# Performance work log

Measured on AMD Instinct MI355X. Metric: run time of the kernel, lower is better.

Reference implementation:

```python
import jax, jax.numpy as jnp
import numpy as np

B = 32768; NF = 8; E = 16; V = 100000; D = 4
IN = 2 * NF * E          # 256 = id_dims + agn_dims
FCN = [256, 128, 64]
DIMS = [IN] + FCN
EPS = 1e-5               # BatchNorm1d eps


def setup_inputs() -> dict:
    ks = jax.random.split(jax.random.key(0), 64)
    inp = {
        'id_idx': jax.random.randint(ks[0], (B, NF), 0, V),
        'agn_idx': jax.random.randint(ks[1], (B, NF), 0, V),
        'domain_id': jax.random.randint(ks[2], (B,), 0, D),
        'id_tables': jax.random.normal(ks[3], (NF, V, E), dtype=jnp.float32) * 0.01,
        'agn_tables': jax.random.normal(ks[4], (NF, V, E), dtype=jnp.float32) * 0.01,
    }
    k = 5
    for i in range(len(FCN)):
        din, dout = DIMS[i], DIMS[i + 1]
        inp[f'mlp_W{i}'] = jax.random.normal(ks[k], (D, din, dout), dtype=jnp.float32) / np.sqrt(din).astype(np.float32); k += 1
        inp[f'mlp_b{i}'] = jnp.zeros((D, dout), jnp.float32)
        inp[f'bn_g{i}'] = jnp.ones((D, dout), jnp.float32)
        inp[f'bn_b{i}'] = jnp.zeros((D, dout), jnp.float32)
        inp[f'gate_W1_{i}'] = jax.random.normal(ks[k], (D, IN, dout), dtype=jnp.float32) / np.sqrt(IN).astype(np.float32); k += 1
        inp[f'gate_b1_{i}'] = jnp.zeros((D, dout), jnp.float32)
        inp[f'gate_W2_{i}'] = jax.random.normal(ks[k], (D, dout, dout), dtype=jnp.float32) / np.sqrt(dout).astype(np.float32); k += 1
        inp[f'gate_b2_{i}'] = jnp.zeros((D, dout), jnp.float32)
    inp['fin_W'] = jax.random.normal(ks[k], (D, DIMS[-1], 1), dtype=jnp.float32) / np.sqrt(DIMS[-1]).astype(np.float32)
    inp['fin_b'] = jnp.zeros((D, 1), jnp.float32)
    return inp


def _embed(tables, idx):
    # tables [NF,V,E], idx [B,NF] -> [B, NF*E] (per-feature lookup then concat)
    g = tables[jnp.arange(NF)[None, :], idx]            # [B,NF,E]
    return g.reshape(idx.shape[0], NF * E)


def _ppnet(id_tables, agn_tables, mlp_W, mlp_b, bn_g, bn_b, gW1, gb1, gW2, gb2,
           fin_W, fin_b, id_idx, agn_idx, domain_id):
    id_x = _embed(id_tables, id_idx)                    # [B, 128]
    agn_x = _embed(agn_tables, agn_idx)                 # [B, 128]
    # gate_input = cat(id_x, agn_x.detach())
    gate_in = jnp.concatenate([id_x, jax.lax.stop_gradient(agn_x)], axis=1)  # [B, IN]
    h = None
    for i in range(len(FCN)):
        # GateNU: Linear->ReLU->Linear->2*sigmoid, broadcast over D domain towers
        g1 = jax.nn.relu(jnp.einsum('bi,dio->dbo', gate_in, gW1[i]) + gb1[i][:, None, :])
        gate = 2.0 * jax.nn.sigmoid(jnp.einsum('dbo,dop->dbp', g1, gW2[i]) + gb2[i][:, None, :])
        # MLP layer: Linear -> BatchNorm1d (train-mode batch stats) -> ReLU
        if h is None:
            h = jnp.einsum('bi,dio->dbo', gate_in, mlp_W[i]) + mlp_b[i][:, None, :]
        else:
            h = jnp.einsum('dbi,dio->dbo', h, mlp_W[i]) + mlp_b[i][:, None, :]
        mu = h.mean(axis=1, keepdims=True)
        var = h.var(axis=1, keepdims=True)              # biased, matches torch BN training
        h = (h - mu) * jax.lax.rsqrt(var + EPS) * bn_g[i][:, None, :] + bn_b[i][:, None, :]
        h = jax.nn.relu(h)
        h = h * gate
    out = jax.nn.sigmoid(jnp.einsum('dbh,dho->dbo', h, fin_W) + fin_b[:, None, :])  # [D,B,1]
    out = out[:, :, 0]                                  # [D,B]
    # torch.where masked-select chain == gather the row of the assigned domain
    return out[domain_id, jnp.arange(out.shape[1])]     # [B]


def reference(id_idx, agn_idx, domain_id, id_tables, agn_tables,
              mlp_W0, mlp_b0, bn_g0, bn_b0, gate_W1_0, gate_b1_0, gate_W2_0, gate_b2_0,
              mlp_W1, mlp_b1, bn_g1, bn_b1, gate_W1_1, gate_b1_1, gate_W2_1, gate_b2_1,
              mlp_W2, mlp_b2, bn_g2, bn_b2, gate_W1_2, gate_b1_2, gate_W2_2, gate_b2_2,
              fin_W, fin_b):
    mlp_W = [mlp_W0, mlp_W1, mlp_W2]; mlp_b = [mlp_b0, mlp_b1, mlp_b2]
    bn_g = [bn_g0, bn_g1, bn_g2]; bn_b = [bn_b0, bn_b1, bn_b2]
    gW1 = [gate_W1_0, gate_W1_1, gate_W1_2]; gb1 = [gate_b1_0, gate_b1_1, gate_b1_2]
    gW2 = [gate_W2_0, gate_W2_1, gate_W2_2]; gb2 = [gate_b2_0, gate_b2_1, gate_b2_2]
    return _ppnet(id_tables, agn_tables, mlp_W, mlp_b, bn_g, bn_b, gW1, gb1, gW2, gb2,
                  fin_W, fin_b, id_idx, agn_idx, domain_id)
```

## Files before the change

### kernel.cpp

```cpp
#include <hip/hip_runtime.h>


typedef __attribute__((ext_vector_type(8))) short short8;
typedef __attribute__((ext_vector_type(4))) float floatx4;

#define BATCH 32768
#define NDOM 4
#define TM 64

__device__ __forceinline__ unsigned short f2b(float f) {
    unsigned u = __float_as_uint(f);
    u += 0x7fffu + ((u >> 16) & 1u);
    return (unsigned short)(u >> 16);
}
__device__ __forceinline__ float b2f(unsigned short h) {
    return __uint_as_float(((unsigned)h) << 16);
}

struct MatDesc { const float* src; unsigned K, N, pfx, total; };
struct PrepArgs { MatDesc m[9]; float* stats; unsigned statsN; unsigned grand; };

__global__ __launch_bounds__(256) void prep_k(PrepArgs a, unsigned short* __restrict__ wt) {
    unsigned e = blockIdx.x * 256 + threadIdx.x;
    if (e < a.statsN) a.stats[e] = 0.f;
    if (e >= a.grand) return;
    int j = 0;
    while (j < 8 && e >= a.m[j].pfx + a.m[j].total) j++;
    const unsigned K = a.m[j].K, N = a.m[j].N;
    const unsigned local = e - a.m[j].pfx;
    const unsigned kn = K * N;
    const unsigned d = local / kn;
    const unsigned r2 = local - d * kn;
    const unsigned n = r2 / K;
    const unsigned k = r2 - n * K;
    wt[e] = f2b(a.m[j].src[((long long)d * K + k) * N + n]);
}

__global__ __launch_bounds__(256) void embed_k(const int* __restrict__ idi, const int* __restrict__ agi,
                                               const float* __restrict__ idt, const float* __restrict__ agt,
                                               unsigned short* __restrict__ gin) {
    int t = blockIdx.x * 256 + threadIdx.x;
    int b = t >> 4, slot = t & 15;
    int f = slot & 7;
    const int* ip = (slot < 8) ? idi : agi;
    const float* tab = (slot < 8) ? idt : agt;
    int ix = ip[b * 8 + f];
    const float* src = tab + ((long long)f * 100000 + ix) * 16;
    unsigned short tmp[16];
#pragma unroll
    for (int j = 0; j < 16; j++) tmp[j] = f2b(src[j]);
    unsigned short* dst = gin + (long long)b * 256 + slot * 16;
    *(uint4*)dst = *(const uint4*)tmp;
    *(uint4*)(dst + 8) = *(const uint4*)(tmp + 8);
}

template <int N, int KX>
__global__ __launch_bounds__(256, 2) void stats_k(
    const unsigned short* __restrict__ X, int ginMode,
    const unsigned short* __restrict__ Wm,
    float* __restrict__ gsum, float* __restrict__ gssq) {
    constexpr int GX = KX / 8;
    constexpr int NW = N / 4, CT = NW / 16;
    __shared__ __align__(16) unsigned short tA[TM * KX];
    const int t = threadIdx.x;
    const int d = blockIdx.y;
    const int m0 = blockIdx.x * TM;
    const unsigned short* Xp = X + ((long long)(ginMode ? 0 : d * BATCH) + m0) * KX;
#pragma unroll
    for (int r = 0; r < TM * GX / 256; r++) {
        int idx = r * 256 + t;
        int m = idx / GX, j = idx % GX;
        uint4 v = *(const uint4*)(Xp + (long long)m * KX + j * 8);
        *(uint4*)&tA[(m * GX + (j ^ (m & 7))) * 8] = v;
    }
    __syncthreads();
    const int w = t >> 6, lane = t & 63, lrow = lane & 15, lq = lane >> 4;
    const int n0w = w * NW;
    const unsigned short* Wp = Wm + ((long long)d * N + n0w) * KX;
    floatx4 acc[4][CT];
#pragma unroll
    for (int rt = 0; rt < 4; rt++)
#pragma unroll
        for (int ct = 0; ct < CT; ct++) acc[rt][ct] = (floatx4)(0.f);
#pragma unroll
    for (int k0 = 0; k0 < KX; k0 += 32) {
        short8 a[4], b[CT];
#pragma unroll
        for (int rt = 0; rt < 4; rt++) {
            int m = rt * 16 + lrow;
            a[rt] = *(const short8*)&tA[(m * GX + (((k0 >> 3) | lq) ^ (m & 7))) * 8];
        }
#pragma unroll
        for (int ct = 0; ct < CT; ct++)
            b[ct] = *(const short8*)(Wp + (long long)(ct * 16 + lrow) * KX + k0 + lq * 8);
#pragma unroll
        for (int rt = 0; rt < 4; rt++)
#pragma unroll
            for (int ct = 0; ct < CT; ct++)
                acc[rt][ct] = __builtin_amdgcn_mfma_f32_16x16x32_bf16(a[rt], b[ct], acc[rt][ct], 0, 0, 0);
    }
#pragma unroll
    for (int ct = 0; ct < CT; ct++) {
        float s = 0.f, ss = 0.f;
#pragma unroll
        for (int rt = 0; rt < 4; rt++)
#pragma unroll
            for (int r = 0; r < 4; r++) { float v = acc[rt][ct][r]; s += v; ss += v * v; }
        s += __shfl_down(s, 32); ss += __shfl_down(ss, 32);
        s += __shfl_down(s, 16); ss += __shfl_down(ss, 16);
        if (lane < 16) {
            atomicAdd(&gsum[d * N + n0w + ct * 16 + lane], s);
            atomicAdd(&gssq[d * N + n0w + ct * 16 + lane], ss);
        }
    }
}

__global__ void fin_k(const float* __restrict__ gsum, const float* __restrict__ gssq,
                      const float* __restrict__ gma, const float* __restrict__ bta,
                      float* __restrict__ SC, float* __restrict__ SH, int total, float invB) {
    int i = blockIdx.x * blockDim.x + threadIdx.x;
    if (i >= total) return;
    float ma = gsum[i] * invB;
    float var = gssq[i] * invB - ma * ma;
    float rs = rsqrtf(var + 1e-5f);
    float sc = rs * gma[i];
    SC[i] = sc;
    SH[i] = bta[i] - ma * sc;
}

template <int N, int KX, bool RESTAGE, bool FINAL>
__global__ __launch_bounds__(256, 2) void fused_k(
    const unsigned short* __restrict__ gin,
    const unsigned short* __restrict__ Xh,
    const unsigned short* __restrict__ W1,
    const unsigned short* __restrict__ W2,
    const unsigned short* __restrict__ Wm,
    const float* __restrict__ gb1, const float* __restrict__ gb2,
    const float* __restrict__ SC, const float* __restrict__ SH,
    unsigned short* __restrict__ Xn,
    const int* __restrict__ dom, const float* __restrict__ fw,
    const float* __restrict__ fb, float* __restrict__ outp) {
    constexpr int GG = N / 8;
    constexpr int GX = KX / 8;
    constexpr int NW = N / 4, CT = NW / 16;
    __shared__ __align__(16) unsigned short tA[TM * 256];
    __shared__ __align__(16) unsigned short g1b[TM * N];
    const int t = threadIdx.x;
    const int d = blockIdx.y;
    const int m0 = blockIdx.x * TM;
    const int w = t >> 6, lane = t & 63, lrow = lane & 15, lq = lane >> 4;
    const int n0w = w * NW;

    {
        const unsigned short* Gp = gin + (long long)m0 * 256;
#pragma unroll
        for (int r = 0; r < 8; r++) {
            int idx = r * 256 + t;
            int m = idx >> 5, j = idx & 31;
            uint4 v = *(const uint4*)(Gp + (long long)m * 256 + j * 8);
            *(uint4*)&tA[((m << 5) + (j ^ (m & 7))) * 8] = v;
        }
    }
    __syncthreads();

    floatx4 acc1[4][CT];
#pragma unroll
    for (int rt = 0; rt < 4; rt++)
#pragma unroll
        for (int ct = 0; ct < CT; ct++) acc1[rt][ct] = (floatx4)(0.f);
    const unsigned short* W1p = W1 + ((long long)d * N + n0w) * 256;
#pragma unroll
    for (int k0 = 0; k0 < 256; k0 += 32) {
        short8 a[4], b[CT];
#pragma unroll
        for (int rt = 0; rt < 4; rt++) {
            int m = rt * 16 + lrow;
            a[rt] = *(const short8*)&tA[((m << 5) + (((k0 >> 3) | lq) ^ (m & 7))) * 8];
        }
#pragma unroll
        for (int ct = 0; ct < CT; ct++)
            b[ct] = *(const short8*)(W1p + (long long)(ct * 16 + lrow) * 256 + k0 + lq * 8);
#pragma unroll
        for (int rt = 0; rt < 4; rt++)
#pragma unroll
            for (int ct = 0; ct < CT; ct++)
                acc1[rt][ct] = __builtin_amdgcn_mfma_f32_16x16x32_bf16(a[rt], b[ct], acc1[rt][ct], 0, 0, 0);
    }
#pragma unroll
    for (int ct = 0; ct < CT; ct++) {
        int n = n0w + ct * 16 + lrow;
        float bs = gb1[d * N + n];
        int jj = n >> 3, sub = n & 7;
#pragma unroll
        for (int rt = 0; rt < 4; rt++)
#pragma unroll
            for (int r = 0; r < 4; r++) {
                int m = rt * 16 + lq * 4 + r;
                g1b[(m * GG + (jj ^ (m & 7))) * 8 + sub] = f2b(fmaxf(acc1[rt][ct][r] + bs, 0.f));
            }
    }
    __syncthreads();

    floatx4 acc2[4][CT];
#pragma unroll
    for (int rt = 0; rt < 4; rt++)
#pragma unroll
        for (int ct = 0; ct < CT; ct++) acc2[rt][ct] = (floatx4)(0.f);
    const unsigned short* W2p = W2 + ((long long)d * N + n0w) * N;
#pragma unroll
    for (int k0 = 0; k0 < N; k0 += 32) {
        short8 a[4], b[CT];
#pragma unroll
        for (int rt = 0; rt < 4; rt++) {
            int m = rt * 16 + lrow;
            a[rt] = *(const short8*)&g1b[(m * GG + (((k0 >> 3) | lq) ^ (m & 7))) * 8];
        }
#pragma unroll
        for (int ct = 0; ct < CT; ct++)
            b[ct] = *(const short8*)(W2p + (long long)(ct * 16 + lrow) * N + k0 + lq * 8);
#pragma unroll
        for (int rt = 0; rt < 4; rt++)
#pragma unroll
            for (int ct = 0; ct < CT; ct++)
                acc2[rt][ct] = __builtin_amdgcn_mfma_f32_16x16x32_bf16(a[rt], b[ct], acc2[rt][ct], 0, 0, 0);
    }
    float gate[4][CT][4];
#pragma unroll
    for (int ct = 0; ct < CT; ct++) {
        int n = n0w + ct * 16 + lrow;
        float bs = gb2[d * N + n];
#pragma unroll
        for (int rt = 0; rt < 4; rt++)
#pragma unroll
            for (int r = 0; r < 4; r++)
                gate[rt][ct][r] = 2.f / (1.f + __expf(-(acc2[rt][ct][r] + bs)));
    }

    if (RESTAGE) {
        const unsigned short* Xp = Xh + ((long long)d * BATCH + m0) * KX;
#pragma unroll
        for (int r = 0; r < TM * GX / 256; r++) {
            int idx = r * 256 + t;
            int m = idx / GX, j = idx % GX;
            uint4 v = *(const uint4*)(Xp + (long long)m * KX + j * 8);
            *(uint4*)&tA[(m * GX + (j ^ (m & 7))) * 8] = v;
        }
    }
    __syncthreads();

    floatx4 acch[4][CT];
#pragma unroll
    for (int rt = 0; rt < 4; rt++)
#pragma unroll
        for (int ct = 0; ct < CT; ct++) acch[rt][ct] = (floatx4)(0.f);
    const unsigned short* Wmp = Wm + ((long long)d * N + n0w) * KX;
#pragma unroll
    for (int k0 = 0; k0 < KX; k0 += 32) {
        short8 a[4], b[CT];
#pragma unroll
        for (int rt = 0; rt < 4; rt++) {
            int m = rt * 16 + lrow;
            a[rt] = *(const short8*)&tA[(m * GX + (((k0 >> 3) | lq) ^ (m & 7))) * 8];
        }
#pragma unroll
        for (int ct = 0; ct < CT; ct++)
            b[ct] = *(const short8*)(Wmp + (long long)(ct * 16 + lrow) * KX + k0 + lq * 8);
#pragma unroll
        for (int rt = 0; rt < 4; rt++)
#pragma unroll
            for (int ct = 0; ct < CT; ct++)
                acch[rt][ct] = __builtin_amdgcn_mfma_f32_16x16x32_bf16(a[rt], b[ct], acch[rt][ct], 0, 0, 0);
    }
#pragma unroll
    for (int ct = 0; ct < CT; ct++) {
        int n = n0w + ct * 16 + lrow;
        float sc = SC[d * N + n], sh = SH[d * N + n];
#pragma unroll
        for (int rt = 0; rt < 4; rt++)
#pragma unroll
            for (int r = 0; r < 4; r++) {
                int m = rt * 16 + lq * 4 + r;
                float v = fmaxf(acch[rt][ct][r] * sc + sh, 0.f) * gate[rt][ct][r];
                g1b[m * N + n] = f2b(v);
            }
    }
    __syncthreads();

    if (!FINAL) {
        unsigned short* Op = Xn + ((long long)d * BATCH + m0) * N;
#pragma unroll
        for (int r = 0; r < TM * GG / 256; r++) {
            int idx = r * 256 + t;
            int m = idx / GG, j = idx % GG;
            *(uint4*)(Op + (long long)m * N + j * 8) = *(const uint4*)&g1b[(m * GG + j) * 8];
        }
    } else {
        int m = t >> 2, q = t & 3;
        const float* fwp = fw + d * 64;
        float s = 0.f;
#pragma unroll
        for (int k = 0; k < 16; k++) s += b2f(g1b[m * 64 + q * 16 + k]) * fwp[q * 16 + k];
        s += __shfl_down(s, 1);
        s += __shfl_down(s, 2);
        if (q == 0) {
            int b = m0 + m;
            if (dom[b] == d) outp[b] = 1.f / (1.f + __expf(-(s + fb[d])));
        }
    }
}

extern "C" void kernel_launch(void* const* d_in, const int* in_sizes, int n_in,
                              void* d_out, int out_size, void* d_ws, size_t ws_size,
                              hipStream_t stream) {
    const int B = BATCH, D = NDOM;

    const int* id_idx = (const int*)d_in[0];
    const int* agn_idx = (const int*)d_in[1];
    const int* dom = (const int*)d_in[2];
    const float* id_t = (const float*)d_in[3];
    const float* agn_t = (const float*)d_in[4];
    const float *mlpW[3], *bng[3], *bnb[3], *gW1[3], *gb1[3], *gW2[3], *gb2[3];
    for (int i = 0; i < 3; i++) {
        int b0 = 5 + i * 8;
        mlpW[i] = (const float*)d_in[b0 + 0];
        bng[i] = (const float*)d_in[b0 + 2];
        bnb[i] = (const float*)d_in[b0 + 3];
        gW1[i] = (const float*)d_in[b0 + 4];
        gb1[i] = (const float*)d_in[b0 + 5];
        gW2[i] = (const float*)d_in[b0 + 6];
        gb2[i] = (const float*)d_in[b0 + 7];
    }
    const float* finW = (const float*)d_in[29];
    const float* finb = (const float*)d_in[30];

    char* wsc = (char*)d_ws;
    size_t off = 0;
    auto alloc = [&](size_t bytes) -> char* {
        char* p = wsc + off;
        off = (off + bytes + 255) & ~(size_t)255;
        return p;
    };

    struct { const float* src; int K, N; } mats[9] = {
        {mlpW[0], 256, 256}, {gW1[0], 256, 256}, {gW2[0], 256, 256},
        {mlpW[1], 256, 128}, {gW1[1], 256, 128}, {gW2[1], 128, 128},
        {mlpW[2], 128, 64},  {gW1[2], 256, 64},  {gW2[2], 64, 64}};
    unsigned pfx[10];
    pfx[0] = 0;
    for (int j = 0; j < 9; j++) pfx[j + 1] = pfx[j] + 4u * mats[j].K * mats[j].N;

    unsigned short* wt = (unsigned short*)alloc((size_t)pfx[9] * 2);
    unsigned short* gin = (unsigned short*)alloc((size_t)B * 256 * 2);
    float* stats = (float*)alloc((size_t)3 * 2 * D * 256 * 4);
    float* scsh = (float*)alloc((size_t)3 * 2 * D * 256 * 4);
    unsigned short* X1 = (unsigned short*)alloc((size_t)D * B * 256 * 2);
    unsigned short* X2 = (unsigned short*)alloc((size_t)D * B * 128 * 2);

    PrepArgs pa;
    for (int j = 0; j < 9; j++) {
        pa.m[j].src = mats[j].src;
        pa.m[j].K = (unsigned)mats[j].K;
        pa.m[j].N = (unsigned)mats[j].N;
        pa.m[j].pfx = pfx[j];
        pa.m[j].total = 4u * mats[j].K * mats[j].N;
    }
    pa.stats = stats;
    pa.statsN = 3 * 2 * D * 256;
    pa.grand = pfx[9];

    const float invB = 1.f / (float)B;
    dim3 gs(B / TM, D);

    prep_k<<<dim3((pfx[9] + 255) / 256), 256, 0, stream>>>(pa, wt);
    embed_k<<<dim3(B * 16 / 256), 256, 0, stream>>>(id_idx, agn_idx, id_t, agn_t, gin);

    float* gsum0 = stats + 0 * 2 * D * 256; float* gssq0 = gsum0 + D * 256;
    float* gsum1 = stats + 1 * 2 * D * 256; float* gssq1 = gsum1 + D * 256;
    float* gsum2 = stats + 2 * 2 * D * 256; float* gssq2 = gsum2 + D * 256;
    float* SC0 = scsh + 0 * 2 * D * 256; float* SH0 = SC0 + D * 256;
    float* SC1 = scsh + 1 * 2 * D * 256; float* SH1 = SC1 + D * 256;
    float* SC2 = scsh + 2 * 2 * D * 256; float* SH2 = SC2 + D * 256;

    stats_k<256, 256><<<gs, 256, 0, stream>>>(gin, 1, wt + pfx[0], gsum0, gssq0);
    fin_k<<<(D * 256 + 255) / 256, 256, 0, stream>>>(gsum0, gssq0, bng[0], bnb[0], SC0, SH0, D * 256, invB);
    fused_k<256, 256, false, false><<<gs, 256, 0, stream>>>(
        gin, gin, wt + pfx[1], wt + pfx[2], wt + pfx[0], gb1[0], gb2[0], SC0, SH0,
        X1, nullptr, nullptr, nullptr, nullptr);

    stats_k<128, 256><<<gs, 256, 0, stream>>>(X1, 0, wt + pfx[3], gsum1, gssq1);
    fin_k<<<(D * 128 + 255) / 256, 256, 0, stream>>>(gsum1, gssq1, bng[1], bnb[1], SC1, SH1, D * 128, invB);
    fused_k<128, 256, true, false><<<gs, 256, 0, stream>>>(
        gin, X1, wt + pfx[4], wt + pfx[5], wt + pfx[3], gb1[1], gb2[1], SC1, SH1,
        X2, nullptr, nullptr, nullptr, nullptr);

    stats_k<64, 128><<<gs, 256, 0, stream>>>(X2, 0, wt + pfx[6], gsum2, gssq2);
    fin_k<<<(D * 64 + 255) / 256, 256, 0, stream>>>(gsum2, gssq2, bng[2], bnb[2], SC2, SH2, D * 64, invB);
    fused_k<64, 128, true, true><<<gs, 256, 0, stream>>>(
        gin, X2, wt + pfx[7], wt + pfx[8], wt + pfx[6], gb1[2], gb2[2], SC2, SH2,
        nullptr, dom, finW, finb, (float*)d_out);
}
```

Before: 506.7 us.

## Fuse next-layer BN statistics and BN finalize into fused layer kernels

Folds the per-layer BatchNorm statistics GEMM for layers 1 and 2 into the previous layer's fused kernel, which now runs the next layer's pre-BN matmul on the output tile still in LDS and accumulates sums via shared-memory atomics before global atomics. BN scale/shift finalization moves into each fused kernel's prologue, and the separate stats and fin kernels for later layers are removed. This avoids re-reading X1/X2 from memory and cuts several launches. In exchange, the fused kernels reuse one shared buffer with extra barriers, pack gates into bf16 registers, and raise launch bounds to 3 blocks per SM, which adds work per block and register pressure.

```diff
diff --git a/kernel.cpp b/kernel.cpp
--- a/kernel.cpp
+++ b/kernel.cpp
@@ -54,18 +54,16 @@
     *(uint4*)(dst + 8) = *(const uint4*)(tmp + 8);
 }
 
-template <int N, int KX>
-__global__ __launch_bounds__(256, 2) void stats_k(
-    const unsigned short* __restrict__ X, int ginMode,
+__global__ __launch_bounds__(256, 3) void stats_k(
+    const unsigned short* __restrict__ X,
     const unsigned short* __restrict__ Wm,
     float* __restrict__ gsum, float* __restrict__ gssq) {
-    constexpr int GX = KX / 8;
-    constexpr int NW = N / 4, CT = NW / 16;
+    constexpr int N = 256, KX = 256, GX = KX / 8, CT = 4;
     __shared__ __align__(16) unsigned short tA[TM * KX];
     const int t = threadIdx.x;
     const int d = blockIdx.y;
     const int m0 = blockIdx.x * TM;
-    const unsigned short* Xp = X + ((long long)(ginMode ? 0 : d * BATCH) + m0) * KX;
+    const unsigned short* Xp = X + (long long)m0 * KX;
 #pragma unroll
     for (int r = 0; r < TM * GX / 256; r++) {
         int idx = r * 256 + t;
@@ -75,7 +73,7 @@
     }
     __syncthreads();
     const int w = t >> 6, lane = t & 63, lrow = lane & 15, lq = lane >> 4;
-    const int n0w = w * NW;
+    const int n0w = w * 64;
     const unsigned short* Wp = Wm + ((long long)d * N + n0w) * KX;
     floatx4 acc[4][CT];
 #pragma unroll
@@ -115,41 +113,43 @@
     }
 }
 
-__global__ void fin_k(const float* __restrict__ gsum, const float* __restrict__ gssq,
-                      const float* __restrict__ gma, const float* __restrict__ bta,
-                      float* __restrict__ SC, float* __restrict__ SH, int total, float invB) {
-    int i = blockIdx.x * blockDim.x + threadIdx.x;
-    if (i >= total) return;
-    float ma = gsum[i] * invB;
-    float var = gssq[i] * invB - ma * ma;
-    float rs = rsqrtf(var + 1e-5f);
-    float sc = rs * gma[i];
-    SC[i] = sc;
-    SH[i] = bta[i] - ma * sc;
-}
-
-template <int N, int KX, bool RESTAGE, bool FINAL>
-__global__ __launch_bounds__(256, 2) void fused_k(
+template <int N, int KX, int NN, bool GINH, bool FINAL>
+__global__ __launch_bounds__(256, 3) void fused_k(
     const unsigned short* __restrict__ gin,
     const unsigned short* __restrict__ Xh,
     const unsigned short* __restrict__ W1,
     const unsigned short* __restrict__ W2,
     const unsigned short* __restrict__ Wm,
+    const unsigned short* __restrict__ WmN,
     const float* __restrict__ gb1, const float* __restrict__ gb2,
-    const float* __restrict__ SC, const float* __restrict__ SH,
+    const float* __restrict__ gsum, const float* __restrict__ gssq,
+    const float* __restrict__ gma, const float* __restrict__ bta,
+    float* __restrict__ gsumN, float* __restrict__ gssqN,
     unsigned short* __restrict__ Xn,
     const int* __restrict__ dom, const float* __restrict__ fw,
-    const float* __restrict__ fb, float* __restrict__ outp) {
-    constexpr int GG = N / 8;
+    const float* __restrict__ fb, float* __restrict__ outp, float invB) {
+    constexpr int GGn = N / 8;
     constexpr int GX = KX / 8;
-    constexpr int NW = N / 4, CT = NW / 16;
-    __shared__ __align__(16) unsigned short tA[TM * 256];
-    __shared__ __align__(16) unsigned short g1b[TM * N];
+    constexpr int CT = N / 64;
+    constexpr int CTn = (NN > 0) ? (NN / 64) : 1;
+    __shared__ __align__(16) unsigned short buf[TM * 256];
+    __shared__ float sSC[N], sSH[N];
+    __shared__ float sSum[NN > 0 ? NN : 1], sSsq[NN > 0 ? NN : 1];
+
     const int t = threadIdx.x;
     const int d = blockIdx.y;
     const int m0 = blockIdx.x * TM;
     const int w = t >> 6, lane = t & 63, lrow = lane & 15, lq = lane >> 4;
-    const int n0w = w * NW;
+    const int n0w = w * (N / 4);
+
+    if (t < N) {
+        float ma = gsum[d * N + t] * invB;
+        float var = gssq[d * N + t] * invB - ma * ma;
+        float sc = rsqrtf(var + 1e-5f) * gma[d * N + t];
+        sSC[t] = sc;
+        sSH[t] = bta[d * N + t] - ma * sc;
+    }
+    if (NN > 0 && t < NN) { sSum[t] = 0.f; sSsq[t] = 0.f; }
 
     {
         const unsigned short* Gp = gin + (long long)m0 * 256;
@@ -158,7 +158,7 @@
             int idx = r * 256 + t;
             int m = idx >> 5, j = idx & 31;
             uint4 v = *(const uint4*)(Gp + (long long)m * 256 + j * 8);
-            *(uint4*)&tA[((m << 5) + (j ^ (m & 7))) * 8] = v;
+            *(uint4*)&buf[((m << 5) + (j ^ (m & 7))) * 8] = v;
         }
     }
     __syncthreads();
@@ -168,24 +168,27 @@
     for (int rt = 0; rt < 4; rt++)
 #pragma unroll
         for (int ct = 0; ct < CT; ct++) acc1[rt][ct] = (floatx4)(0.f);
-    const unsigned short* W1p = W1 + ((long long)d * N + n0w) * 256;
-#pragma unroll
-    for (int k0 = 0; k0 < 256; k0 += 32) {
-        short8 a[4], b[CT];
-#pragma unroll
-        for (int rt = 0; rt < 4; rt++) {
-            int m = rt * 16 + lrow;
-            a[rt] = *(const short8*)&tA[((m << 5) + (((k0 >> 3) | lq) ^ (m & 7))) * 8];
-        }
-#pragma unroll
-        for (int ct = 0; ct < CT; ct++)
-            b[ct] = *(const short8*)(W1p + (long long)(ct * 16 + lrow) * 256 + k0 + lq * 8);
-#pragma unroll
-        for (int rt = 0; rt < 4; rt++)
+    {
+        const unsigned short* W1p = W1 + ((long long)d * N + n0w) * 256;
+#pragma unroll
+        for (int k0 = 0; k0 < 256; k0 += 32) {
+            short8 a[4], b[CT];
+#pragma unroll
+            for (int rt = 0; rt < 4; rt++) {
+                int m = rt * 16 + lrow;
+                a[rt] = *(const short8*)&buf[((m << 5) + (((k0 >> 3) | lq) ^ (m & 7))) * 8];
+            }
 #pragma unroll
             for (int ct = 0; ct < CT; ct++)
-                acc1[rt][ct] = __builtin_amdgcn_mfma_f32_16x16x32_bf16(a[rt], b[ct], acc1[rt][ct], 0, 0, 0);
-    }
+                b[ct] = *(const short8*)(W1p + (long long)(ct * 16 + lrow) * 256 + k0 + lq * 8);
+#pragma unroll
+            for (int rt = 0; rt < 4; rt++)
+#pragma unroll
+                for (int ct = 0; ct < CT; ct++)
+                    acc1[rt][ct] = __builtin_amdgcn_mfma_f32_16x16x32_bf16(a[rt], b[ct], acc1[rt][ct], 0, 0, 0);
+        }
+    }
+    __syncthreads();
 #pragma unroll
     for (int ct = 0; ct < CT; ct++) {
         int n = n0w + ct * 16 + lrow;
@@ -196,7 +199,7 @@
 #pragma unroll
             for (int r = 0; r < 4; r++) {
                 int m = rt * 16 + lq * 4 + r;
-                g1b[(m * GG + (jj ^ (m & 7))) * 8 + sub] = f2b(fmaxf(acc1[rt][ct][r] + bs, 0.f));
+                buf[(m * GGn + (jj ^ (m & 7))) * 8 + sub] = f2b(fmaxf(acc1[rt][ct][r] + bs, 0.f));
             }
     }
     __syncthreads();
@@ -206,44 +209,51 @@
     for (int rt = 0; rt < 4; rt++)
 #pragma unroll
         for (int ct = 0; ct < CT; ct++) acc2[rt][ct] = (floatx4)(0.f);
-    const unsigned short* W2p = W2 + ((long long)d * N + n0w) * N;
-#pragma unroll
-    for (int k0 = 0; k0 < N; k0 += 32) {
-        short8 a[4], b[CT];
-#pragma unroll
-        for (int rt = 0; rt < 4; rt++) {
-            int m = rt * 16 + lrow;
-            a[rt] = *(const short8*)&g1b[(m * GG + (((k0 >> 3) | lq) ^ (m & 7))) * 8];
-        }
-#pragma unroll
-        for (int ct = 0; ct < CT; ct++)
-            b[ct] = *(const short8*)(W2p + (long long)(ct * 16 + lrow) * N + k0 + lq * 8);
-#pragma unroll
-        for (int rt = 0; rt < 4; rt++)
+    {
+        const unsigned short* W2p = W2 + ((long long)d * N + n0w) * N;
+#pragma unroll
+        for (int k0 = 0; k0 < N; k0 += 32) {
+            short8 a[4], b[CT];
+#pragma unroll
+            for (int rt = 0; rt < 4; rt++) {
+                int m = rt * 16 + lrow;
+                a[rt] = *(const short8*)&buf[(m * GGn + ((((k0 >> 3) | lq)) ^ (m & 7))) * 8];
+            }
 #pragma unroll
             for (int ct = 0; ct < CT; ct++)
-                acc2[rt][ct] = __builtin_amdgcn_mfma_f32_16x16x32_bf16(a[rt], b[ct], acc2[rt][ct], 0, 0, 0);
-    }
-    float gate[4][CT][4];
+                b[ct] = *(const short8*)(W2p + (long long)(ct * 16 + lrow) * N + k0 + lq * 8);
+#pragma unroll
+            for (int rt = 0; rt < 4; rt++)
+#pragma unroll
+                for (int ct = 0; ct < CT; ct++)
+                    acc2[rt][ct] = __builtin_amdgcn_mfma_f32_16x16x32_bf16(a[rt], b[ct], acc2[rt][ct], 0, 0, 0);
+        }
+    }
+    unsigned gatep[4][CT][2];
 #pragma unroll
     for (int ct = 0; ct < CT; ct++) {
         int n = n0w + ct * 16 + lrow;
         float bs = gb2[d * N + n];
 #pragma unroll
-        for (int rt = 0; rt < 4; rt++)
-#pragma unroll
-            for (int r = 0; r < 4; r++)
-                gate[rt][ct][r] = 2.f / (1.f + __expf(-(acc2[rt][ct][r] + bs)));
-    }
-
-    if (RESTAGE) {
-        const unsigned short* Xp = Xh + ((long long)d * BATCH + m0) * KX;
+        for (int rt = 0; rt < 4; rt++) {
+            float g0 = 2.f / (1.f + __expf(-(acc2[rt][ct][0] + bs)));
+            float g1 = 2.f / (1.f + __expf(-(acc2[rt][ct][1] + bs)));
+            float g2 = 2.f / (1.f + __expf(-(acc2[rt][ct][2] + bs)));
+            float g3 = 2.f / (1.f + __expf(-(acc2[rt][ct][3] + bs)));
+            gatep[rt][ct][0] = (unsigned)f2b(g0) | ((unsigned)f2b(g1) << 16);
+            gatep[rt][ct][1] = (unsigned)f2b(g2) | ((unsigned)f2b(g3) << 16);
+        }
+    }
+    __syncthreads();
+
+    {
+        const unsigned short* Xp = Xh + ((long long)(GINH ? 0 : d * BATCH) + m0) * KX;
 #pragma unroll
         for (int r = 0; r < TM * GX / 256; r++) {
             int idx = r * 256 + t;
             int m = idx / GX, j = idx % GX;
             uint4 v = *(const uint4*)(Xp + (long long)m * KX + j * 8);
-            *(uint4*)&tA[(m * GX + (j ^ (m & 7))) * 8] = v;
+            *(uint4*)&buf[(m * GX + (j ^ (m & 7))) * 8] = v;
         }
     }
     __syncthreads();
@@ -253,58 +263,117 @@
     for (int rt = 0; rt < 4; rt++)
 #pragma unroll
         for (int ct = 0; ct < CT; ct++) acch[rt][ct] = (floatx4)(0.f);
-    const unsigned short* Wmp = Wm + ((long long)d * N + n0w) * KX;
-#pragma unroll
-    for (int k0 = 0; k0 < KX; k0 += 32) {
-        short8 a[4], b[CT];
-#pragma unroll
-        for (int rt = 0; rt < 4; rt++) {
-            int m = rt * 16 + lrow;
-            a[rt] = *(const short8*)&tA[(m * GX + (((k0 >> 3) | lq) ^ (m & 7))) * 8];
-        }
-#pragma unroll
-        for (int ct = 0; ct < CT; ct++)
-            b[ct] = *(const short8*)(Wmp + (long long)(ct * 16 + lrow) * KX + k0 + lq * 8);
-#pragma unroll
-        for (int rt = 0; rt < 4; rt++)
+    {
+        const unsigned short* Wmp = Wm + ((long long)d * N + n0w) * KX;
+#pragma unroll
+        for (int k0 = 0; k0 < KX; k0 += 32) {
+            short8 a[4], b[CT];
+#pragma unroll
+            for (int rt = 0; rt < 4; rt++) {
+                int m = rt * 16 + lrow;
+                a[rt] = *(const short8*)&buf[(m * GX + (((k0 >> 3) | lq) ^ (m & 7))) * 8];
+            }
 #pragma unroll
             for (int ct = 0; ct < CT; ct++)
-                acch[rt][ct] = __builtin_amdgcn_mfma_f32_16x16x32_bf16(a[rt], b[ct], acch[rt][ct], 0, 0, 0);
-    }
+                b[ct] = *(const short8*)(Wmp + (long long)(ct * 16 + lrow) * KX + k0 + lq * 8);
+#pragma unroll
+            for (int rt = 0; rt < 4; rt++)
+#pragma unroll
+                for (int ct = 0; ct < CT; ct++)
+                    acch[rt][ct] = __builtin_amdgcn_mfma_f32_16x16x32_bf16(a[rt], b[ct], acch[rt][ct], 0, 0, 0);
+        }
+    }
+    __syncthreads();
+
 #pragma unroll
     for (int ct = 0; ct < CT; ct++) {
         int n = n0w + ct * 16 + lrow;
-        float sc = SC[d * N + n], sh = SH[d * N + n];
-#pragma unroll
-        for (int rt = 0; rt < 4; rt++)
+        float sc = sSC[n], sh = sSH[n];
+        int jj = n >> 3, sub = n & 7;
+#pragma unroll
+        for (int rt = 0; rt < 4; rt++) {
+            float gv[4] = {b2f((unsigned short)(gatep[rt][ct][0] & 0xffff)),
+                           b2f((unsigned short)(gatep[rt][ct][0] >> 16)),
+                           b2f((unsigned short)(gatep[rt][ct][1] & 0xffff)),
+                           b2f((unsigned short)(gatep[rt][ct][1] >> 16))};
 #pragma unroll
             for (int r = 0; r < 4; r++) {
                 int m = rt * 16 + lq * 4 + r;
-                float v = fmaxf(acch[rt][ct][r] * sc + sh, 0.f) * gate[rt][ct][r];
-                g1b[m * N + n] = f2b(v);
-            }
+                float v = fmaxf(acch[rt][ct][r] * sc + sh, 0.f) * gv[r];
+                buf[(m * GGn + (jj ^ (m & 7))) * 8 + sub] = f2b(v);
+            }
+        }
     }
     __syncthreads();
 
     if (!FINAL) {
         unsigned short* Op = Xn + ((long long)d * BATCH + m0) * N;
 #pragma unroll
-        for (int r = 0; r < TM * GG / 256; r++) {
+        for (int r = 0; r < TM * GGn / 256; r++) {
             int idx = r * 256 + t;
-            int m = idx / GG, j = idx % GG;
-            *(uint4*)(Op + (long long)m * N + j * 8) = *(const uint4*)&g1b[(m * GG + j) * 8];
+            int m = idx / GGn, j = idx % GGn;
+            *(uint4*)(Op + (long long)m * N + j * 8) = *(const uint4*)&buf[(m * GGn + (j ^ (m & 7))) * 8];
         }
     } else {
         int m = t >> 2, q = t & 3;
         const float* fwp = fw + d * 64;
         float s = 0.f;
 #pragma unroll
-        for (int k = 0; k < 16; k++) s += b2f(g1b[m * 64 + q * 16 + k]) * fwp[q * 16 + k];
+        for (int k = 0; k < 16; k++) {
+            int c = q * 16 + k;
+            s += b2f(buf[(m * 8 + ((c >> 3) ^ (m & 7))) * 8 + (c & 7)]) * fwp[c];
+        }
         s += __shfl_down(s, 1);
         s += __shfl_down(s, 2);
         if (q == 0) {
             int b = m0 + m;
             if (dom[b] == d) outp[b] = 1.f / (1.f + __expf(-(s + fb[d])));
+        }
+    }
+
+    if (NN > 0) {
+        const int n0wN = w * (NN / 4);
+        floatx4 accs[4][CTn];
+#pragma unroll
+        for (int rt = 0; rt < 4; rt++)
+#pragma unroll
+            for (int ct = 0; ct < CTn; ct++) accs[rt][ct] = (floatx4)(0.f);
+        const unsigned short* Wnp = WmN + ((long long)d * NN + n0wN) * N;
+#pragma unroll
+        for (int k0 = 0; k0 < N; k0 += 32) {
+            short8 a[4], b[CTn];
+#pragma unroll
+            for (int rt = 0; rt < 4; rt++) {
+                int m = rt * 16 + lrow;
+                a[rt] = *(const short8*)&buf[(m * GGn + (((k0 >> 3) | lq) ^ (m & 7))) * 8];
+            }
+#pragma unroll
+            for (int ct = 0; ct < CTn; ct++)
+                b[ct] = *(const short8*)(Wnp + (long long)(ct * 16 + lrow) * N + k0 + lq * 8);
+#pragma unroll
+            for (int rt = 0; rt < 4; rt++)
+#pragma unroll
+                for (int ct = 0; ct < CTn; ct++)
+                    accs[rt][ct] = __builtin_amdgcn_mfma_f32_16x16x32_bf16(a[rt], b[ct], accs[rt][ct], 0, 0, 0);
+        }
+#pragma unroll
+        for (int ct = 0; ct < CTn; ct++) {
+            float s = 0.f, ss = 0.f;
+#pragma unroll
+            for (int rt = 0; rt < 4; rt++)
+#pragma unroll
+                for (int r = 0; r < 4; r++) { float v = accs[rt][ct][r]; s += v; ss += v * v; }
+            s += __shfl_down(s, 32); ss += __shfl_down(ss, 32);
+            s += __shfl_down(s, 16); ss += __shfl_down(ss, 16);
+            if (lane < 16) {
+                atomicAdd(&sSum[n0wN + ct * 16 + lane], s);
+                atomicAdd(&sSsq[n0wN + ct * 16 + lane], ss);
+            }
+        }
+        __syncthreads();
+        if (t < NN) {
+            atomicAdd(&gsumN[d * NN + t], sSum[t]);
+            atomicAdd(&gssqN[d * NN + t], sSsq[t]);
         }
     }
 }
@@ -352,7 +421,6 @@
     unsigned short* wt = (unsigned short*)alloc((size_t)pfx[9] * 2);
     unsigned short* gin = (unsigned short*)alloc((size_t)B * 256 * 2);
     float* stats = (float*)alloc((size_t)3 * 2 * D * 256 * 4);
-    float* scsh = (float*)alloc((size_t)3 * 2 * D * 256 * 4);
     unsigned short* X1 = (unsigned short*)alloc((size_t)D * B * 256 * 2);
     unsigned short* X2 = (unsigned short*)alloc((size_t)D * B * 128 * 2);
 
@@ -377,25 +445,21 @@
     float* gsum0 = stats + 0 * 2 * D * 256; float* gssq0 = gsum0 + D * 256;
     float* gsum1 = stats + 1 * 2 * D * 256; float* gssq1 = gsum1 + D * 256;
     float* gsum2 = stats + 2 * 2 * D * 256; float* gssq2 = gsum2 + D * 256;
-    float* SC0 = scsh + 0 * 2 * D * 256; float* SH0 = SC0 + D * 256;
-    float* SC1 = scsh + 1 * 2 * D * 256; float* SH1 = SC1 + D * 256;
-    float* SC2 = scsh + 2 * 2 * D * 256; float* SH2 = SC2 + D * 256;
-
-    stats_k<256, 256><<<gs, 256, 0, stream>>>(gin, 1, wt + pfx[0], gsum0, gssq0);
-    fin_k<<<(D * 256 + 255) / 256, 256, 0, stream>>>(gsum0, gssq0, bng[0], bnb[0], SC0, SH0, D * 256, invB);
-    fused_k<256, 256, false, false><<<gs, 256, 0, stream>>>(
-        gin, gin, wt + pfx[1], wt + pfx[2], wt + pfx[0], gb1[0], gb2[0], SC0, SH0,
-        X1, nullptr, nullptr, nullptr, nullptr);
-
-    stats_k<128, 256><<<gs, 256, 0, stream>>>(X1, 0, wt + pfx[3], gsum1, gssq1);
-    fin_k<<<(D * 128 + 255) / 256, 256, 0, stream>>>(gsum1, gssq1, bng[1], bnb[1], SC1, SH1, D * 128, invB);
-    fused_k<128, 256, true, false><<<gs, 256, 0, stream>>>(
-        gin, X1, wt + pfx[4], wt + pfx[5], wt + pfx[3], gb1[1], gb2[1], SC1, SH1,
-        X2, nullptr, nullptr, nullptr, nullptr);
-
-    stats_k<64, 128><<<gs, 256, 0, stream>>>(X2, 0, wt + pfx[6], gsum2, gssq2);
-    fin_k<<<(D * 64 + 255) / 256, 256, 0, stream>>>(gsum2, gssq2, bng[2], bnb[2], SC2, SH2, D * 64, invB);
-    fused_k<64, 128, true, true><<<gs, 256, 0, stream>>>(
-        gin, X2, wt + pfx[7], wt + pfx[8], wt + pfx[6], gb1[2], gb2[2], SC2, SH2,
-        nullptr, dom, finW, finb, (float*)d_out);
-}
+
+    stats_k<<<gs, 256, 0, stream>>>(gin, wt + pfx[0], gsum0, gssq0);
+
+    fused_k<256, 256, 128, true, false><<<gs, 256, 0, stream>>>(
+        gin, gin, wt + pfx[1], wt + pfx[2], wt + pfx[0], wt + pfx[3],
+        gb1[0], gb2[0], gsum0, gssq0, bng[0], bnb[0], gsum1, gssq1,
+        X1, nullptr, nullptr, nullptr, nullptr, invB);
+
+    fused_k<128, 256, 64, false, false><<<gs, 256, 0, stream>>>(
+        gin, X1, wt + pfx[4], wt + pfx[5], wt + pfx[3], wt + pfx[6],
+        gb1[1], gb2[1], gsum1, gssq1, bng[1], bnb[1], gsum2, gssq2,
+        X2, nullptr, nullptr, nullptr, nullptr, invB);
+
+    fused_k<64, 128, 0, false, true><<<gs, 256, 0, stream>>>(
+        gin, X2, wt + pfx[7], wt + pfx[8], wt + pfx[6], nullptr,
+        gb1[2], gb2[2], gsum2, gssq2, bng[2], bnb[2], nullptr, nullptr,
+        nullptr, dom, finW, finb, (float*)d_out, invB);
+}
```

Result: slower. 590.1 us (+16.5%).
